# Kernel tuning notes

Measured on AMD Instinct MI355X. Metric: run time of the kernel, lower is better.

The kernel has to match this reference:

```python
import jax, jax.numpy as jnp
import numpy as np

C = 256        # in_channels
HEADS = 8
HD = 64        # dim_heads
INNER = HEADS * HD   # 512
G = 32         # norm_groups
FF = 4 * INNER # 2048
EPS = 1e-5


def setup_inputs() -> dict:
    key = jax.random.key(0)
    ks = jax.random.split(key, 12)
    r = lambda k, shp: jax.random.normal(k, shp, jnp.float32) * 0.02
    return {
        "x": jax.random.normal(ks[0], (1, C, 16, 16, 16), jnp.float32),
        "gn_g": jnp.ones((C,), jnp.float32),
        "gn_b": jnp.zeros((C,), jnp.float32),
        "w_in": r(ks[1], (INNER, C)),   # Conv3d 1x1x1 as (out,in) matrix
        "b_in": jnp.zeros((INNER,), jnp.float32),
        "wq": r(ks[2], (INNER, INNER)),
        "wk": r(ks[3], (INNER, INNER)),
        "wv": r(ks[4], (INNER, INNER)),
        "ln1_g": jnp.ones((INNER,), jnp.float32),
        "ln1_b": jnp.zeros((INNER,), jnp.float32),
        "ff_w1": r(ks[5], (FF, INNER)),
        "ff_b1": jnp.zeros((FF,), jnp.float32),
        "ff_w2": r(ks[6], (INNER, FF)),
        "ff_b2": jnp.zeros((INNER,), jnp.float32),
        "ln2_g": jnp.ones((INNER,), jnp.float32),
        "ln2_b": jnp.zeros((INNER,), jnp.float32),
        "w_out": r(ks[7], (C, INNER)),  # Conv3d 1x1x1 back to C
        "b_out": jnp.zeros((C,), jnp.float32),
    }


def _group_norm(x, g, b):
    # x: (B,C,D,H,W), G groups, normalize over (C//G, D, H, W)
    B, Cc, D, H, W = x.shape
    xr = x.reshape(B, G, Cc // G, D, H, W)
    mu = jnp.mean(xr, axis=(2, 3, 4, 5), keepdims=True)
    var = jnp.var(xr, axis=(2, 3, 4, 5), keepdims=True)
    xr = (xr - mu) * jax.lax.rsqrt(var + EPS)
    xn = xr.reshape(B, Cc, D, H, W)
    return xn * g[None, :, None, None, None] + b[None, :, None, None, None]


def _layer_norm(x, g, b):
    mu = jnp.mean(x, axis=-1, keepdims=True)
    var = jnp.var(x, axis=-1, keepdims=True)
    return (x - mu) * jax.lax.rsqrt(var + EPS) * g + b


def reference(x, gn_g, gn_b, w_in, b_in, wq, wk, wv, ln1_g, ln1_b,
              ff_w1, ff_b1, ff_w2, ff_b2, ln2_g, ln2_b, w_out, b_out):
    B, Cc, D, H, W = x.shape
    x_in = x
    # GroupNorm + proj_in (1x1x1 conv == channel matmul)
    h = _group_norm(x, gn_g, gn_b)
    t = jnp.einsum('bcdhw,oc->bodhw', h, w_in) + b_in[None, :, None, None, None]
    N = D * H * W
    t = t.reshape(B, INNER, N).transpose(0, 2, 1)  # (B, N, INNER)

    # self-attention (manual einsum softmax einsum)
    q = (t @ wq.T).reshape(B, N, HEADS, HD)
    k = (t @ wk.T).reshape(B, N, HEADS, HD)
    v = (t @ wv.T).reshape(B, N, HEADS, HD)
    scale = HD ** (-0.5)
    scores = jnp.einsum('bihd,bjhd->bhij', q, k) * scale  # (B,H,N,N)
    attn = jax.nn.softmax(scores, axis=-1)
    o = jnp.einsum('bhij,bjhd->bihd', attn, v).reshape(B, N, INNER)
    # out_proj is Identity (q_dim == inner_dim), dropout=0
    t = _layer_norm(o + t, ln1_g, ln1_b)

    # FeedForward: Linear -> GELU (erf) -> Linear
    ff = jax.nn.gelu(t @ ff_w1.T + ff_b1, approximate=False) @ ff_w2.T + ff_b2
    t = _layer_norm(ff + t, ln2_g, ln2_b)

    # proj_out + residual
    y = t.transpose(0, 2, 1).reshape(B, INNER, D, H, W)
    out = jnp.einsum('bidhw,oi->bodhw', y, w_out) + b_out[None, :, None, None, None]
    return out + x_in
```

## Files before the change

### kernel.cpp

```cpp
#include <hip/hip_runtime.h>
#include <hip/hip_bf16.h>

typedef unsigned short u16;
typedef __attribute__((ext_vector_type(8))) short short8;
typedef __attribute__((ext_vector_type(4))) float floatx4;

#define LOG2E 1.44269504088896f
#define CEXP (0.125f * LOG2E)

static __device__ __forceinline__ u16 f2b(float f) {
  union { float f; unsigned u; } v; v.f = f;
  unsigned r = v.u + 0x7fffu + ((v.u >> 16) & 1u);
  return (u16)(r >> 16);
}
static __device__ __forceinline__ float b2f(u16 b) {
  union { float f; unsigned u; } v; v.u = ((unsigned)b) << 16;
  return v.f;
}
static __device__ __forceinline__ void async16(const u16* g, u16* l) {
  __builtin_amdgcn_global_load_lds(
      (const __attribute__((address_space(1))) unsigned int*)g,
      (__attribute__((address_space(3))) unsigned int*)l, 16, 0, 0);
}
static __device__ __forceinline__ float fexp2(float x) {
  return __builtin_amdgcn_exp2f(x);
}

__global__ __launch_bounds__(256) void f2b_all(
    const float* __restrict__ s0, const float* __restrict__ s1, const float* __restrict__ s2,
    const float* __restrict__ s3, const float* __restrict__ s4, const float* __restrict__ s5,
    const float* __restrict__ s6, const float* __restrict__ x,
    u16* __restrict__ d_win, u16* __restrict__ d_qkv, u16* __restrict__ d_f1,
    u16* __restrict__ d_f2, u16* __restrict__ d_wout, float2* __restrict__ cstats) {
  if (blockIdx.x >= 12288) {
    int c = blockIdx.x - 12288;
    const float4* p4 = (const float4*)(x + (size_t)c * 4096);
    float s = 0.f, ss = 0.f;
#pragma unroll
    for (int j = 0; j < 4; j++) {
      float4 v = p4[j * 256 + threadIdx.x];
      s += v.x + v.y + v.z + v.w;
      ss += v.x * v.x + v.y * v.y + v.z * v.z + v.w * v.w;
    }
    for (int m = 1; m < 64; m <<= 1) { s += __shfl_xor(s, m); ss += __shfl_xor(ss, m); }
    __shared__ float sb[8];
    int w = threadIdx.x >> 6;
    if ((threadIdx.x & 63) == 0) { sb[w * 2] = s; sb[w * 2 + 1] = ss; }
    __syncthreads();
    if (threadIdx.x == 0)
      cstats[c] = float2{sb[0] + sb[2] + sb[4] + sb[6], sb[1] + sb[3] + sb[5] + sb[7]};
    return;
  }
  int i = blockIdx.x * 256 + threadIdx.x;
  if (i < 131072) { d_win[i] = f2b(s0[i]); return; }
  i -= 131072;
  if (i < 262144) { d_qkv[i] = f2b(s1[i]); return; }
  i -= 262144;
  if (i < 262144) { d_qkv[262144 + i] = f2b(s2[i]); return; }
  i -= 262144;
  if (i < 262144) { d_qkv[524288 + i] = f2b(s3[i]); return; }
  i -= 262144;
  if (i < 1048576) { d_f1[i] = f2b(s4[i]); return; }
  i -= 1048576;
  if (i < 1048576) { d_f2[i] = f2b(s5[i]); return; }
  i -= 1048576;
  d_wout[i] = f2b(s6[i]);
}

__global__ __launch_bounds__(256) void gn_apply(const float* __restrict__ x, const float2* __restrict__ cstats,
                                                const float* __restrict__ gg, const float* __restrict__ gb,
                                                u16* __restrict__ hn) {
  int idx = blockIdx.x * 256 + threadIdx.x;
  int c = idx >> 12, n = idx & 4095;
  int g = c >> 3;
  float s = 0.f, ss = 0.f;
#pragma unroll
  for (int j = 0; j < 8; j++) {
    float2 p = cstats[g * 8 + j];
    s += p.x; ss += p.y;
  }
  float mu = s / 32768.f;
  float rs = rsqrtf(ss / 32768.f - mu * mu + 1e-5f);
  float v = (x[idx] - mu) * rs * gg[c] + gb[c];
  hn[(size_t)n * 256 + c] = f2b(v);
}

#define FLAG_BIAS 1
#define FLAG_GELU 2
#define FLAG_C16 8
#define FLAG_FINAL 32
#define FLAG_CZ 64

__global__ __launch_bounds__(256) void gemm_bt(
    const u16* __restrict__ A, const u16* __restrict__ B, const float* __restrict__ bias,
    float* __restrict__ C32, u16* __restrict__ C16, const float* __restrict__ resid,
    int M, int N, int K, int flags) {
  __shared__ u16 As[128 * 64];
  __shared__ u16 Bs[64 * 64];
  const int t = threadIdx.x;
  const int lane = t & 63;
  const int w = t >> 6;
  const int ln = lane & 15;
  const int quad = lane >> 4;
  const int m0 = blockIdx.x * 128;
  const int n0 = blockIdx.y * 64;
  const int wm = (w >> 1) * 64;
  const int wn = (w & 1) * 32;

  floatx4 acc[4][2];
#pragma unroll
  for (int i = 0; i < 4; i++)
#pragma unroll
    for (int j = 0; j < 2; j++) acc[i][j] = floatx4{0.f, 0.f, 0.f, 0.f};

  for (int k0 = 0; k0 < K; k0 += 64) {
    __syncthreads();
#pragma unroll
    for (int i = 0; i < 4; ++i) {
      int s = i * 256 + t;
      int row = s >> 3;
      int kb = (s & 7) ^ (row & 7);
      async16(A + (size_t)(m0 + row) * K + k0 + kb * 8, &As[(i * 256 + (t & ~63)) * 8]);
    }
#pragma unroll
    for (int i = 0; i < 2; ++i) {
      int s = i * 256 + t;
      int row = s >> 3;
      int kb = (s & 7) ^ (row & 7);
      async16(B + (size_t)(n0 + row) * K + k0 + kb * 8, &Bs[(i * 256 + (t & ~63)) * 8]);
    }
    __syncthreads();
#pragma unroll
    for (int ksi = 0; ksi < 2; ksi++) {
      short8 af[4], bfr[2];
      int kb = ksi * 4 + quad;
#pragma unroll
      for (int i = 0; i < 4; i++) {
        int m = wm + i * 16 + ln;
        af[i] = *(const short8*)&As[(m * 8 + (kb ^ (m & 7))) * 8];
      }
#pragma unroll
      for (int j = 0; j < 2; j++) {
        int n = wn + j * 16 + ln;
        bfr[j] = *(const short8*)&Bs[(n * 8 + (kb ^ (n & 7))) * 8];
      }
#pragma unroll
      for (int i = 0; i < 4; i++)
#pragma unroll
        for (int j = 0; j < 2; j++)
          acc[i][j] = __builtin_amdgcn_mfma_f32_16x16x32_bf16(af[i], bfr[j], acc[i][j], 0, 0, 0);
    }
  }

#pragma unroll
  for (int i = 0; i < 4; i++) {
#pragma unroll
    for (int j = 0; j < 2; j++) {
      int n = n0 + wn + j * 16 + ln;
      float bv = (flags & FLAG_BIAS) ? bias[n] : 0.f;
#pragma unroll
      for (int r = 0; r < 4; r++) {
        int m = m0 + wm + i * 16 + quad * 4 + r;
        float v = acc[i][j][r] + bv;
        if (flags & FLAG_C16) C16[(size_t)m * N + n] = f2b(v);
        if (flags & FLAG_FINAL)
          C32[(size_t)m * N + n] = v + bias[m] + resid[(size_t)m * N + n];
      }
    }
  }
}

__global__ __launch_bounds__(256) void gemm_big(
    const u16* __restrict__ A, const u16* __restrict__ B, const float* __restrict__ bias,
    u16* __restrict__ C16, int M, int N, int K, int flags) {
  __shared__ u16 As[128 * 64];
  __shared__ u16 Bs[128 * 64];
  const int t = threadIdx.x;
  const int lane = t & 63;
  const int w = t >> 6;
  const int ln = lane & 15;
  const int quad = lane >> 4;
  const int m0 = blockIdx.x * 128;
  const int n0 = blockIdx.y * 128;
  const int wm = (w >> 1) * 64;
  const int wn = (w & 1) * 64;
  const int kper = K / gridDim.z;
  const int kbeg = blockIdx.z * kper;

  floatx4 acc[4][4];
#pragma unroll
  for (int i = 0; i < 4; i++)
#pragma unroll
    for (int j = 0; j < 4; j++) acc[i][j] = floatx4{0.f, 0.f, 0.f, 0.f};

  for (int k0 = kbeg; k0 < kbeg + kper; k0 += 64) {
    __syncthreads();
#pragma unroll
    for (int i = 0; i < 4; ++i) {
      int s = i * 256 + t;
      int row = s >> 3;
      int kb = (s & 7) ^ (row & 7);
      async16(A + (size_t)(m0 + row) * K + k0 + kb * 8, &As[(i * 256 + (t & ~63)) * 8]);
      async16(B + (size_t)(n0 + row) * K + k0 + kb * 8, &Bs[(i * 256 + (t & ~63)) * 8]);
    }
    __syncthreads();
#pragma unroll
    for (int ksi = 0; ksi < 2; ksi++) {
      short8 af[4], bfr[4];
      int kb = ksi * 4 + quad;
#pragma unroll
      for (int i = 0; i < 4; i++) {
        int m = wm + i * 16 + ln;
        af[i] = *(const short8*)&As[(m * 8 + (kb ^ (m & 7))) * 8];
        int n = wn + i * 16 + ln;
        bfr[i] = *(const short8*)&Bs[(n * 8 + (kb ^ (n & 7))) * 8];
      }
#pragma unroll
      for (int i = 0; i < 4; i++)
#pragma unroll
        for (int j = 0; j < 4; j++)
          acc[i][j] = __builtin_amdgcn_mfma_f32_16x16x32_bf16(af[i], bfr[j], acc[i][j], 0, 0, 0);
    }
  }

  u16* Cdst = (flags & FLAG_CZ) ? C16 + (size_t)blockIdx.z * M * N : C16;
#pragma unroll
  for (int i = 0; i < 4; i++) {
#pragma unroll
    for (int j = 0; j < 4; j++) {
      int n = n0 + wn + j * 16 + ln;
      float bv = ((flags & FLAG_BIAS) && blockIdx.z == 0) ? bias[n] : 0.f;
#pragma unroll
      for (int r = 0; r < 4; r++) {
        int m = m0 + wm + i * 16 + quad * 4 + r;
        float v = acc[i][j][r] + bv;
        if (flags & FLAG_GELU) v = 0.5f * v * (1.f + erff(v * 0.70710678118f));
        Cdst[(size_t)m * N + n] = f2b(v);
      }
    }
  }
}

__global__ __launch_bounds__(256) void gemm_qkv(
    const u16* __restrict__ A, const u16* __restrict__ B,
    u16* __restrict__ Cq, u16* __restrict__ Ck, u16* __restrict__ CvT,
    int M, int K) {
  __shared__ u16 As[64 * 64];
  __shared__ u16 Bs[128 * 64];
  const int t = threadIdx.x;
  const int lane = t & 63;
  const int w = t >> 6;
  const int ln = lane & 15;
  const int quad = lane >> 4;
  const int m0 = blockIdx.x * 64;
  const int n0 = blockIdx.y * 128;
  const int wm = (w >> 1) * 32;
  const int wn = (w & 1) * 64;

  floatx4 acc[2][4];
#pragma unroll
  for (int i = 0; i < 2; i++)
#pragma unroll
    for (int j = 0; j < 4; j++) acc[i][j] = floatx4{0.f, 0.f, 0.f, 0.f};

  for (int k0 = 0; k0 < K; k0 += 64) {
    __syncthreads();
#pragma unroll
    for (int i = 0; i < 2; ++i) {
      int s = i * 256 + t;
      int row = s >> 3;
      int kb = (s & 7) ^ (row & 7);
      async16(A + (size_t)(m0 + row) * K + k0 + kb * 8, &As[(i * 256 + (t & ~63)) * 8]);
    }
#pragma unroll
    for (int i = 0; i < 4; ++i) {
      int s = i * 256 + t;
      int row = s >> 3;
      int kb = (s & 7) ^ (row & 7);
      async16(B + (size_t)(n0 + row) * K + k0 + kb * 8, &Bs[(i * 256 + (t & ~63)) * 8]);
    }
    __syncthreads();
#pragma unroll
    for (int ksi = 0; ksi < 2; ksi++) {
      short8 af[2], bfr[4];
      int kb = ksi * 4 + quad;
#pragma unroll
      for (int i = 0; i < 2; i++) {
        int m = wm + i * 16 + ln;
        af[i] = *(const short8*)&As[(m * 8 + (kb ^ (m & 7))) * 8];
      }
#pragma unroll
      for (int j = 0; j < 4; j++) {
        int n = wn + j * 16 + ln;
        bfr[j] = *(const short8*)&Bs[(n * 8 + (kb ^ (n & 7))) * 8];
      }
#pragma unroll
      for (int i = 0; i < 2; i++)
#pragma unroll
        for (int j = 0; j < 4; j++)
          acc[i][j] = __builtin_amdgcn_mfma_f32_16x16x32_bf16(af[i], bfr[j], acc[i][j], 0, 0, 0);
    }
  }

#pragma unroll
  for (int i = 0; i < 2; i++) {
#pragma unroll
    for (int j = 0; j < 4; j++) {
      int n = n0 + wn + j * 16 + ln;
#pragma unroll
      for (int r = 0; r < 4; r++) {
        int m = m0 + wm + i * 16 + quad * 4 + r;
        float v = acc[i][j][r];
        if (n < 512) Cq[(size_t)m * 512 + n] = f2b(v * CEXP);
        else if (n < 1024) Ck[(size_t)m * 512 + (n - 512)] = f2b(v);
        else CvT[(size_t)(n - 1024) * M + m] = f2b(v);
      }
    }
  }
}

__global__ __launch_bounds__(256, 4) void attn_kernel(
    const u16* __restrict__ Q, const u16* __restrict__ Km, const u16* __restrict__ VT,
    u16* __restrict__ Opart, float* __restrict__ ML, int Nseq, int kvLen) {
  __shared__ u16 Ks[2][64 * 64];
  __shared__ u16 Vs[2][64 * 64];
  __shared__ u16 Ps[4 * 32 * 64];
  const int t = threadIdx.x;
  const int lane = t & 63;
  const int w = t >> 6;
  const int ln = lane & 15;
  const int quad = lane >> 4;
  const int h = blockIdx.y;
  const int q0 = blockIdx.x * 128;
  const int split = blockIdx.z;
  const int kvbase = split * kvLen;
  u16* Opw = Opart + (size_t)split * Nseq * 512;
  u16* Pw = &Ps[w * 32 * 64];

  short8 qf[2][2];
#pragma unroll
  for (int qt = 0; qt < 2; qt++)
#pragma unroll
    for (int ksi = 0; ksi < 2; ksi++)
      qf[qt][ksi] = *(const short8*)&Q[(size_t)(q0 + w * 32 + qt * 16 + ln) * 512 + h * 64 + ksi * 32 + quad * 8];

  floatx4 accO[2][4];
#pragma unroll
  for (int qt = 0; qt < 2; qt++)
#pragma unroll
    for (int td = 0; td < 4; td++) accO[qt][td] = floatx4{0.f, 0.f, 0.f, 0.f};
  float lsum[2] = {0.f, 0.f};

  const int ntiles = kvLen >> 6;
#pragma unroll
  for (int i = 0; i < 2; ++i) {
    int s = i * 256 + t;
    int row = s >> 3;
    int kb = (s & 7) ^ (row & 7);
    async16(Km + (size_t)(kvbase + row) * 512 + h * 64 + kb * 8, &Ks[0][(i * 256 + (t & ~63)) * 8]);
    async16(VT + (size_t)(h * 64 + row) * Nseq + kvbase + kb * 8, &Vs[0][(i * 256 + (t & ~63)) * 8]);
  }

  for (int tile = 0; tile < ntiles; ++tile) {
    const int p = tile & 1;
    __syncthreads();
    if (tile + 1 < ntiles) {
      const int kv0 = kvbase + (tile + 1) * 64;
#pragma unroll
      for (int i = 0; i < 2; ++i) {
        int s = i * 256 + t;
        int row = s >> 3;
        int kb = (s & 7) ^ (row & 7);
        async16(Km + (size_t)(kv0 + row) * 512 + h * 64 + kb * 8, &Ks[p ^ 1][(i * 256 + (t & ~63)) * 8]);
        async16(VT + (size_t)(h * 64 + row) * Nseq + kv0 + kb * 8, &Vs[p ^ 1][(i * 256 + (t & ~63)) * 8]);
      }
    }
    const u16* Kc = Ks[p];
    const u16* Vc = Vs[p];

    floatx4 accS[2][4];
#pragma unroll
    for (int qt = 0; qt < 2; qt++)
#pragma unroll
      for (int tj = 0; tj < 4; tj++) accS[qt][tj] = floatx4{0.f, 0.f, 0.f, 0.f};
#pragma unroll
    for (int ksi = 0; ksi < 2; ksi++) {
      int kb = ksi * 4 + quad;
      short8 kf[4];
#pragma unroll
      for (int tj = 0; tj < 4; tj++) {
        int key = tj * 16 + ln;
        kf[tj] = *(const short8*)&Kc[(key * 8 + (kb ^ (key & 7))) * 8];
      }
#pragma unroll
      for (int qt = 0; qt < 2; qt++)
#pragma unroll
        for (int tj = 0; tj < 4; tj++)
          accS[qt][tj] = __builtin_amdgcn_mfma_f32_16x16x32_bf16(kf[tj], qf[qt][ksi], accS[qt][tj], 0, 0, 0);
    }

#pragma unroll
    for (int qt = 0; qt < 2; qt++) {
      int q8 = (qt * 16 + ln) * 8;
#pragma unroll
      for (int tj = 0; tj < 4; tj++) {
        float p0 = fexp2(accS[qt][tj][0]);
        float p1 = fexp2(accS[qt][tj][1]);
        float p2 = fexp2(accS[qt][tj][2]);
        float p3 = fexp2(accS[qt][tj][3]);
        lsum[qt] += (p0 + p1) + (p2 + p3);
        __hip_bfloat162 a01 = __float22bfloat162_rn(float2{p0, p1});
        __hip_bfloat162 a23 = __float22bfloat162_rn(float2{p2, p3});
        uint2 pk;
        pk.x = *(unsigned*)&a01;
        pk.y = *(unsigned*)&a23;
        int kbx = tj * 2 + (quad >> 1);
        *(uint2*)&Pw[(q8 + (kbx ^ (ln & 7))) * 8 + (quad & 1) * 4] = pk;
      }
    }

#pragma unroll
    for (int ksi = 0; ksi < 2; ksi++) {
      int kb = ksi * 4 + quad;
      short8 pf[2];
#pragma unroll
      for (int qt = 0; qt < 2; qt++)
        pf[qt] = *(const short8*)&Pw[((qt * 16 + ln) * 8 + (kb ^ (ln & 7))) * 8];
#pragma unroll
      for (int td = 0; td < 4; td++) {
        int d = td * 16 + ln;
        short8 vf = *(const short8*)&Vc[(d * 8 + (kb ^ (d & 7))) * 8];
#pragma unroll
        for (int qt = 0; qt < 2; qt++)
          accO[qt][td] = __builtin_amdgcn_mfma_f32_16x16x32_bf16(vf, pf[qt], accO[qt][td], 0, 0, 0);
      }
    }
  }

#pragma unroll
  for (int qt = 0; qt < 2; qt++) {
    lsum[qt] += __shfl_xor(lsum[qt], 16);
    lsum[qt] += __shfl_xor(lsum[qt], 32);
  }
#pragma unroll
  for (int qt = 0; qt < 2; qt++) {
    int q = q0 + w * 32 + qt * 16 + ln;
#pragma unroll
    for (int td = 0; td < 4; td++) {
      __hip_bfloat162 p01 = __float22bfloat162_rn(float2{accO[qt][td][0], accO[qt][td][1]});
      __hip_bfloat162 p23 = __float22bfloat162_rn(float2{accO[qt][td][2], accO[qt][td][3]});
      uint2 pk;
      pk.x = *(unsigned*)&p01;
      pk.y = *(unsigned*)&p23;
      *(uint2*)&Opw[(size_t)q * 512 + h * 64 + td * 16 + quad * 4] = pk;
    }
    if (quad == 0)
      ML[((size_t)split * 8 + h) * Nseq + q] = lsum[qt];
  }
}

__global__ __launch_bounds__(256) void ln_attn(
    const u16* __restrict__ Opart, const float* __restrict__ ML,
    const u16* __restrict__ t16, const float* __restrict__ g, const float* __restrict__ be,
    u16* __restrict__ o16) {
  int row = blockIdx.x;
  int t = threadIdx.x;
  size_t base = (size_t)row * 512;
  int c0 = 2 * t;
  int h = c0 >> 6;
  float lt = 0.f;
#pragma unroll
  for (int s = 0; s < 4; s++) lt += ML[((size_t)s * 8 + h) * 4096 + row];
  float a0 = 0.f, a1 = 0.f;
#pragma unroll
  for (int s = 0; s < 4; s++) {
    unsigned oo = *(const unsigned*)&Opart[(size_t)s * 4096 * 512 + base + c0];
    a0 += b2f((u16)(oo & 0xffff));
    a1 += b2f((u16)(oo >> 16));
  }
  unsigned tt = *(const unsigned*)&t16[base + c0];
  float inv = 1.0f / lt;
  float v0 = a0 * inv + b2f((u16)(tt & 0xffff));
  float v1 = a1 * inv + b2f((u16)(tt >> 16));
  float s = v0 + v1, ss = v0 * v0 + v1 * v1;
  for (int m = 1; m < 64; m <<= 1) { s += __shfl_xor(s, m); ss += __shfl_xor(ss, m); }
  __shared__ float sb[8];
  int w = t >> 6;
  if ((t & 63) == 0) { sb[w * 2] = s; sb[w * 2 + 1] = ss; }
  __syncthreads();
  s = sb[0] + sb[2] + sb[4] + sb[6];
  ss = sb[1] + sb[3] + sb[5] + sb[7];
  float mu = s / 512.f;
  float var = ss / 512.f - mu * mu;
  float rs = rsqrtf(var + 1e-5f);
  float2 gv = *(const float2*)&g[c0];
  float2 bv = *(const float2*)&be[c0];
  u16 r0 = f2b((v0 - mu) * rs * gv.x + bv.x);
  u16 r1 = f2b((v1 - mu) * rs * gv.y + bv.y);
  *(unsigned*)&o16[base + c0] = ((unsigned)r1 << 16) | r0;
}

__global__ __launch_bounds__(256) void ln_ff(
    const u16* __restrict__ zp, const u16* __restrict__ u,
    const float* __restrict__ g, const float* __restrict__ be, u16* __restrict__ o16) {
  int row = blockIdx.x;
  int t = threadIdx.x;
  size_t base = (size_t)row * 512;
  int c0 = 2 * t;
  unsigned uu = *(const unsigned*)&u[base + c0];
  float v0 = b2f((u16)(uu & 0xffff));
  float v1 = b2f((u16)(uu >> 16));
#pragma unroll
  for (int z = 0; z < 4; z++) {
    unsigned zz = *(const unsigned*)&zp[(size_t)z * 4096 * 512 + base + c0];
    v0 += b2f((u16)(zz & 0xffff));
    v1 += b2f((u16)(zz >> 16));
  }
  float s = v0 + v1, ss = v0 * v0 + v1 * v1;
  for (int m = 1; m < 64; m <<= 1) { s += __shfl_xor(s, m); ss += __shfl_xor(ss, m); }
  __shared__ float sb[8];
  int w = t >> 6;
  if ((t & 63) == 0) { sb[w * 2] = s; sb[w * 2 + 1] = ss; }
  __syncthreads();
  s = sb[0] + sb[2] + sb[4] + sb[6];
  ss = sb[1] + sb[3] + sb[5] + sb[7];
  float mu = s / 512.f;
  float var = ss / 512.f - mu * mu;
  float rs = rsqrtf(var + 1e-5f);
  float2 gv = *(const float2*)&g[c0];
  float2 bv = *(const float2*)&be[c0];
  u16 r0 = f2b((v0 - mu) * rs * gv.x + bv.x);
  u16 r1 = f2b((v1 - mu) * rs * gv.y + bv.y);
  *(unsigned*)&o16[base + c0] = ((unsigned)r1 << 16) | r0;
}

extern "C" void kernel_launch(void* const* d_in, const int* in_sizes, int n_in,
                              void* d_out, int out_size, void* d_ws, size_t ws_size,
                              hipStream_t stream) {
  const float* x = (const float*)d_in[0];
  const float* gn_g = (const float*)d_in[1];
  const float* gn_b = (const float*)d_in[2];
  const float* w_in = (const float*)d_in[3];
  const float* b_in = (const float*)d_in[4];
  const float* wq = (const float*)d_in[5];
  const float* wk = (const float*)d_in[6];
  const float* wv = (const float*)d_in[7];
  const float* ln1_g = (const float*)d_in[8];
  const float* ln1_b = (const float*)d_in[9];
  const float* ff_w1 = (const float*)d_in[10];
  const float* ff_b1 = (const float*)d_in[11];
  const float* ff_w2 = (const float*)d_in[12];
  const float* ff_b2 = (const float*)d_in[13];
  const float* ln2_g = (const float*)d_in[14];
  const float* ln2_b = (const float*)d_in[15];
  const float* w_out = (const float*)d_in[16];
  const float* b_out = (const float*)d_in[17];
  float* out = (float*)d_out;
  char* ws = (char*)d_ws;

  u16* w_in16 = (u16*)(ws + 0);
  u16* wqkv16 = (u16*)(ws + 262144);
  u16* fw116 = (u16*)(ws + 1835008);
  u16* fw216 = (u16*)(ws + 3932160);
  u16* wout16 = (u16*)(ws + 6029312);
  u16* u16b = (u16*)(ws + 6291456);
  u16* zp = (u16*)(ws + 10485760);
  u16* t16 = (u16*)(ws + 14680064);
  u16* qb = (u16*)(ws + 18874368);
  u16* kb = (u16*)(ws + 23068672);
  u16* vt = (u16*)(ws + 27262976);
  u16* zb = (u16*)(ws + 27262976);
  u16* opart = (u16*)(ws + 31457280);
  u16* g16 = (u16*)(ws + 31457280);
  float* ml = (float*)(ws + 48234496);
  u16* hn = (u16*)(ws + 49283072);
  float2* cstats = (float2*)(ws + 51380224);

  f2b_all<<<12544, 256, 0, stream>>>(w_in, wq, wk, wv, ff_w1, ff_w2, w_out, x,
                                     w_in16, wqkv16, fw116, fw216, wout16, cstats);
  gn_apply<<<4096, 256, 0, stream>>>(x, cstats, gn_g, gn_b, hn);

  gemm_bt<<<dim3(32, 8), 256, 0, stream>>>(hn, w_in16, b_in, nullptr, t16, nullptr,
                                           4096, 512, 256, FLAG_BIAS | FLAG_C16);
  gemm_qkv<<<dim3(64, 12), 256, 0, stream>>>(t16, wqkv16, qb, kb, vt, 4096, 512);
  attn_kernel<<<dim3(32, 8, 4), 256, 0, stream>>>(qb, kb, vt, opart, ml, 4096, 1024);
  ln_attn<<<4096, 256, 0, stream>>>(opart, ml, t16, ln1_g, ln1_b, u16b);
  gemm_big<<<dim3(32, 16), 256, 0, stream>>>(u16b, fw116, ff_b1, g16,
                                             4096, 2048, 512, FLAG_BIAS | FLAG_GELU | FLAG_C16);
  gemm_big<<<dim3(32, 4, 4), 256, 0, stream>>>(g16, fw216, ff_b2, zp,
                                               4096, 512, 2048, FLAG_BIAS | FLAG_CZ);
  ln_ff<<<4096, 256, 0, stream>>>(zp, u16b, ln2_g, ln2_b, zb);
  gemm_bt<<<dim3(2, 64), 256, 0, stream>>>(wout16, zb, b_out, out, nullptr, x,
                                           256, 4096, 512, FLAG_FINAL);
}
```

Baseline: 250.1 us.

## Tile GroupNorm transpose, compute V^T via separate GEMM, single-buffer attention KV

GroupNorm apply now stages a 256-channel by 16-position tile through padded shared memory, so global reads and writes are coalesced instead of writing transposed with stride. The V projection is split out of the fused QKV GEMM into a gemm_bt call computing W_v·T^T, which writes V^T row-contiguously instead of scattering transposed stores. The attention kernel drops double-buffered async K/V prefetch in favour of a single buffer with load-then-sync. That halves K/V shared memory but gives up the overlap of loads with MFMA work.

Result: no change. 245.2 us (-1.9%).

```diff
diff --git a/kernel.cpp b/kernel.cpp
--- a/kernel.cpp
+++ b/kernel.cpp
@@ -70,19 +70,35 @@
 __global__ __launch_bounds__(256) void gn_apply(const float* __restrict__ x, const float2* __restrict__ cstats,
                                                 const float* __restrict__ gg, const float* __restrict__ gb,
                                                 u16* __restrict__ hn) {
-  int idx = blockIdx.x * 256 + threadIdx.x;
-  int c = idx >> 12, n = idx & 4095;
-  int g = c >> 3;
-  float s = 0.f, ss = 0.f;
-#pragma unroll
-  for (int j = 0; j < 8; j++) {
-    float2 p = cstats[g * 8 + j];
-    s += p.x; ss += p.y;
-  }
-  float mu = s / 32768.f;
-  float rs = rsqrtf(ss / 32768.f - mu * mu + 1e-5f);
-  float v = (x[idx] - mu) * rs * gg[c] + gb[c];
-  hn[(size_t)n * 256 + c] = f2b(v);
+  __shared__ float tile[256 * 17];
+  __shared__ float gmu[32], grs[32];
+  int t = threadIdx.x;
+  if (t < 32) {
+    float s = 0.f, ss = 0.f;
+#pragma unroll
+    for (int j = 0; j < 8; j++) { float2 p = cstats[t * 8 + j]; s += p.x; ss += p.y; }
+    float mu = s / 32768.f;
+    gmu[t] = mu;
+    grs[t] = rsqrtf(ss / 32768.f - mu * mu + 1e-5f);
+  }
+  __syncthreads();
+  int n0 = blockIdx.x * 16;
+#pragma unroll
+  for (int j = 0; j < 4; j++) {
+    int c = j * 64 + (t >> 2);
+    int nl = (t & 3) * 4;
+    float4 v = *(const float4*)&x[(size_t)c * 4096 + n0 + nl];
+    float ga = gg[c] * grs[c >> 3];
+    float bb = gb[c] - gmu[c >> 3] * ga;
+    tile[c * 17 + nl + 0] = v.x * ga + bb;
+    tile[c * 17 + nl + 1] = v.y * ga + bb;
+    tile[c * 17 + nl + 2] = v.z * ga + bb;
+    tile[c * 17 + nl + 3] = v.w * ga + bb;
+  }
+  __syncthreads();
+#pragma unroll
+  for (int j = 0; j < 16; j++)
+    hn[(size_t)(n0 + j) * 256 + t] = f2b(tile[t * 17 + j]);
 }
 
 #define FLAG_BIAS 1
@@ -241,10 +257,9 @@
   }
 }
 
-__global__ __launch_bounds__(256) void gemm_qkv(
+__global__ __launch_bounds__(256) void gemm_qk(
     const u16* __restrict__ A, const u16* __restrict__ B,
-    u16* __restrict__ Cq, u16* __restrict__ Ck, u16* __restrict__ CvT,
-    int M, int K) {
+    u16* __restrict__ Cq, u16* __restrict__ Ck, int M, int K) {
   __shared__ u16 As[64 * 64];
   __shared__ u16 Bs[128 * 64];
   const int t = threadIdx.x;
@@ -312,8 +327,7 @@
         int m = m0 + wm + i * 16 + quad * 4 + r;
         float v = acc[i][j][r];
         if (n < 512) Cq[(size_t)m * 512 + n] = f2b(v * CEXP);
-        else if (n < 1024) Ck[(size_t)m * 512 + (n - 512)] = f2b(v);
-        else CvT[(size_t)(n - 1024) * M + m] = f2b(v);
+        else Ck[(size_t)m * 512 + (n - 512)] = f2b(v);
       }
     }
   }
@@ -322,8 +336,8 @@
 __global__ __launch_bounds__(256, 4) void attn_kernel(
     const u16* __restrict__ Q, const u16* __restrict__ Km, const u16* __restrict__ VT,
     u16* __restrict__ Opart, float* __restrict__ ML, int Nseq, int kvLen) {
-  __shared__ u16 Ks[2][64 * 64];
-  __shared__ u16 Vs[2][64 * 64];
+  __shared__ u16 Ks[64 * 64];
+  __shared__ u16 Vs[64 * 64];
   __shared__ u16 Ps[4 * 32 * 64];
   const int t = threadIdx.x;
   const int lane = t & 63;
@@ -351,32 +365,18 @@
     for (int td = 0; td < 4; td++) accO[qt][td] = floatx4{0.f, 0.f, 0.f, 0.f};
   float lsum[2] = {0.f, 0.f};
 
-  const int ntiles = kvLen >> 6;
-#pragma unroll
-  for (int i = 0; i < 2; ++i) {
-    int s = i * 256 + t;
-    int row = s >> 3;
-    int kb = (s & 7) ^ (row & 7);
-    async16(Km + (size_t)(kvbase + row) * 512 + h * 64 + kb * 8, &Ks[0][(i * 256 + (t & ~63)) * 8]);
-    async16(VT + (size_t)(h * 64 + row) * Nseq + kvbase + kb * 8, &Vs[0][(i * 256 + (t & ~63)) * 8]);
-  }
-
-  for (int tile = 0; tile < ntiles; ++tile) {
-    const int p = tile & 1;
-    __syncthreads();
-    if (tile + 1 < ntiles) {
-      const int kv0 = kvbase + (tile + 1) * 64;
-#pragma unroll
-      for (int i = 0; i < 2; ++i) {
-        int s = i * 256 + t;
-        int row = s >> 3;
-        int kb = (s & 7) ^ (row & 7);
-        async16(Km + (size_t)(kv0 + row) * 512 + h * 64 + kb * 8, &Ks[p ^ 1][(i * 256 + (t & ~63)) * 8]);
-        async16(VT + (size_t)(h * 64 + row) * Nseq + kv0 + kb * 8, &Vs[p ^ 1][(i * 256 + (t & ~63)) * 8]);
-      }
-    }
-    const u16* Kc = Ks[p];
-    const u16* Vc = Vs[p];
+  for (int kv = 0; kv < kvLen; kv += 64) {
+    const int kv0 = kvbase + kv;
+    __syncthreads();
+#pragma unroll
+    for (int i = 0; i < 2; ++i) {
+      int s = i * 256 + t;
+      int row = s >> 3;
+      int kb = (s & 7) ^ (row & 7);
+      async16(Km + (size_t)(kv0 + row) * 512 + h * 64 + kb * 8, &Ks[(i * 256 + (t & ~63)) * 8]);
+      async16(VT + (size_t)(h * 64 + row) * Nseq + kv0 + kb * 8, &Vs[(i * 256 + (t & ~63)) * 8]);
+    }
+    __syncthreads();
 
     floatx4 accS[2][4];
 #pragma unroll
@@ -390,7 +390,7 @@
 #pragma unroll
       for (int tj = 0; tj < 4; tj++) {
         int key = tj * 16 + ln;
-        kf[tj] = *(const short8*)&Kc[(key * 8 + (kb ^ (key & 7))) * 8];
+        kf[tj] = *(const short8*)&Ks[(key * 8 + (kb ^ (key & 7))) * 8];
       }
 #pragma unroll
       for (int qt = 0; qt < 2; qt++)
@@ -429,7 +429,7 @@
 #pragma unroll
       for (int td = 0; td < 4; td++) {
         int d = td * 16 + ln;
-        short8 vf = *(const short8*)&Vc[(d * 8 + (kb ^ (d & 7))) * 8];
+        short8 vf = *(const short8*)&Vs[(d * 8 + (kb ^ (d & 7))) * 8];
 #pragma unroll
         for (int qt = 0; qt < 2; qt++)
           accO[qt][td] = __builtin_amdgcn_mfma_f32_16x16x32_bf16(vf, pf[qt], accO[qt][td], 0, 0, 0);
@@ -578,11 +578,13 @@
 
   f2b_all<<<12544, 256, 0, stream>>>(w_in, wq, wk, wv, ff_w1, ff_w2, w_out, x,
                                      w_in16, wqkv16, fw116, fw216, wout16, cstats);
-  gn_apply<<<4096, 256, 0, stream>>>(x, cstats, gn_g, gn_b, hn);
+  gn_apply<<<256, 256, 0, stream>>>(x, cstats, gn_g, gn_b, hn);
 
   gemm_bt<<<dim3(32, 8), 256, 0, stream>>>(hn, w_in16, b_in, nullptr, t16, nullptr,
                                            4096, 512, 256, FLAG_BIAS | FLAG_C16);
-  gemm_qkv<<<dim3(64, 12), 256, 0, stream>>>(t16, wqkv16, qb, kb, vt, 4096, 512);
+  gemm_qk<<<dim3(64, 8), 256, 0, stream>>>(t16, wqkv16, qb, kb, 4096, 512);
+  gemm_bt<<<dim3(4, 64), 256, 0, stream>>>(wqkv16 + 2 * 512 * 512, t16, nullptr, nullptr, vt, nullptr,
+                                           512, 4096, 512, FLAG_C16);
   attn_kernel<<<dim3(32, 8, 4), 256, 0, stream>>>(qb, kb, vt, opart, ml, 4096, 1024);
   ln_attn<<<4096, 256, 0, stream>>>(opart, ml, t16, ln1_g, ln1_b, u16b);
   gemm_big<<<dim3(32, 16), 256, 0, stream>>>(u16b, fw116, ff_b1, g16,
```
